# Optimization experiments

Measured on AMD Instinct MI355X. Metric: run time of the kernel, lower is better.

Reference implementation:

```python
import jax, jax.numpy as jnp
import numpy as np

MAX_CACHE_LEN = 1024
B, S, D, H = 8, 512, 512, 8
DK = D // H


def setup_inputs() -> dict:
    key = jax.random.key(0)
    ks = jax.random.split(key, 11)
    w = lambda k: jax.random.normal(k, (D, D), jnp.float32) * 0.02
    b = lambda k: jax.random.normal(k, (D,), jnp.float32) * 0.02
    return {
        "x": jax.random.normal(ks[0], (B, S, D), jnp.float32),
        "prev_k": jax.random.normal(ks[1], (B, H, MAX_CACHE_LEN, DK), jnp.float32),
        "prev_v": jax.random.normal(ks[2], (B, H, MAX_CACHE_LEN, DK), jnp.float32),
        "Wq": w(ks[3]), "bq": b(ks[4]),
        "Wk": w(ks[5]), "bk": b(ks[6]),
        "Wv": w(ks[7]), "bv": b(ks[8]),
        "Wo": w(ks[9]), "bo": b(ks[10]),
        "offset": MAX_CACHE_LEN,  # cache already full (steady-state streaming)
    }


def reference(x, prev_k, prev_v, Wq, bq, Wk, bk, Wv, bv, Wo, bo, offset):
    Bx, Sx, Dx = x.shape
    Hx = prev_k.shape[1]
    dk = Dx // Hx
    # projections (torch Linear: y = x @ W.T + b), split into heads -> [B,H,S,dk]
    def proj(W, bias):
        return (x @ W.T + bias).reshape(Bx, Sx, Hx, dk).transpose(0, 2, 1, 3)
    q = proj(Wq, bq)
    k = jnp.concatenate([prev_k, proj(Wk, bk)], axis=2)
    v = jnp.concatenate([prev_v, proj(Wv, bv)], axis=2)
    # sliding-window narrow to last MAX_CACHE_LEN keys (static shapes under jit)
    k_full = k.shape[2]
    start = max(0, k_full - MAX_CACHE_LEN)
    k = k[:, :, start:, :]
    v = v[:, :, start:, :]
    k_len = k.shape[2]
    new_offset = min(offset + Sx, MAX_CACHE_LEN)
    # scores [B,H,S,k_len]
    scores = jnp.einsum("bhqd,bhkd->bhqk", q, k) * (dk ** -0.5)
    q_start = new_offset - Sx
    q_idx = jnp.arange(Sx)[:, None] + q_start
    k_idx = jnp.arange(k_len)[None, :]
    mask = q_idx < k_idx  # future keys masked
    scores = jnp.where(mask[None, None], -jnp.inf, scores)
    attn = jax.nn.softmax(scores, axis=-1)
    out = jnp.einsum("bhqk,bhkd->bhqd", attn, v)
    out = out.transpose(0, 2, 1, 3).reshape(Bx, Sx, Dx)
    out = out @ Wo.T + bo
    return out, k, v, jnp.asarray(new_offset, jnp.int64 if jax.config.x64_enabled else jnp.int32)
```

## Files before the change

### kernel.cpp

```cpp
#include <hip/hip_runtime.h>
#include <math.h>

#define B_  8
#define S_  512
#define D_  512
#define H_  8
#define DK_ 64
#define KL_ 1024

typedef __attribute__((ext_vector_type(8))) short bf16x8;
typedef __attribute__((ext_vector_type(4))) float f32x4;

__device__ __forceinline__ unsigned short f2bf(float f) {
    unsigned u = __float_as_uint(f);
    u += 0x7FFF + ((u >> 16) & 1);
    return (unsigned short)(u >> 16);
}
__device__ __forceinline__ unsigned pkbf(float lo, float hi) {
    return __builtin_amdgcn_perm(__float_as_uint(hi), __float_as_uint(lo), 0x07060302u);
}
__device__ __forceinline__ bf16x8 pack8(float4 a, float4 b) {
    union { bf16x8 v; unsigned u[4]; } r;
    r.u[0] = pkbf(a.x, a.y); r.u[1] = pkbf(a.z, a.w);
    r.u[2] = pkbf(b.x, b.y); r.u[3] = pkbf(b.z, b.w);
    return r.v;
}
__device__ __forceinline__ void gld16(const void* g, void* l) {
    __builtin_amdgcn_global_load_lds(
        (const __attribute__((address_space(1))) unsigned int*)g,
        (__attribute__((address_space(3))) unsigned int*)l, 16, 0, 0);
}

__global__ __launch_bounds__(256)
void prep_kernel(const float4* __restrict__ pk, const float4* __restrict__ pv,
                 float4* __restrict__ kout4, float4* __restrict__ vout4,
                 float* __restrict__ off_out) {
    int i = blockIdx.x * 256 + threadIdx.x;
    int bh = i >> 13, r4 = i & 8191;
    kout4[bh * 16384 + r4] = pk[bh * 16384 + 8192 + r4];
    vout4[bh * 16384 + r4] = pv[bh * 16384 + 8192 + r4];
    if (i == 0) off_out[0] = 1024.0f;
}

template<int MODE, int BM>
__device__ __forceinline__
void mfma_gemm_body(const float* __restrict__ A32,
                    const unsigned short* __restrict__ A16,
                    const float* __restrict__ Wf,
                    const float* __restrict__ bias,
                    float* __restrict__ C32, unsigned short* __restrict__ C16) {
    constexpr int MM = BM / 32;
    __shared__ unsigned short As[BM * 32];
    __shared__ unsigned short Bs[64 * 32];
    const int t = threadIdx.x, l = t & 63, w = t >> 6;
    const int m16 = l & 15, quad = l >> 4;
    const int wm = w >> 1, wn = w & 1;
    const int bn = blockIdx.x, bm = blockIdx.y;

    f32x4 acc[MM][2] = {};

    for (int k0 = 0; k0 < 512; k0 += 32) {
        __syncthreads();
        if (MODE == 3) {
            const int h = k0 >> 6, dd0 = k0 & 63;
            const int lr = l >> 2, lc = (l & 3) * 8;
            const unsigned short* Ab =
                A16 + (((bm >> 3) * 8 + h) * 512 + (bm & 7) * 64) * 64 + dd0;
            gld16(Ab + (w * 16 + lr) * 64 + lc, &As[w * 512 + l * 8]);
        } else {
            #pragma unroll
            for (int s = 0; s < BM / 64; ++s) {
                int id = t + s * 256;
                int row = id >> 2, c8 = id & 3;
                const float* src = A32 + (bm * BM + row) * 512 + k0 + c8 * 8;
                float4 v0 = *(const float4*)src;
                float4 v1 = *(const float4*)(src + 4);
                *(bf16x8*)&As[row * 32 + c8 * 8] = pack8(v0, v1);
            }
        }
        {
            int row = t >> 2, c8 = t & 3;
            const float* src = Wf + (bn * 64 + row) * 512 + k0 + c8 * 8;
            float4 v0 = *(const float4*)src;
            float4 v1 = *(const float4*)(src + 4);
            *(bf16x8*)&Bs[row * 32 + c8 * 8] = pack8(v0, v1);
        }
        __syncthreads();

        bf16x8 af[MM], bfr[2];
        #pragma unroll
        for (int mm = 0; mm < MM; ++mm)
            af[mm] = *(const bf16x8*)&As[(wm * (BM / 2) + mm * 16 + m16) * 32 + quad * 8];
        #pragma unroll
        for (int nn = 0; nn < 2; ++nn)
            bfr[nn] = *(const bf16x8*)&Bs[(wn * 32 + nn * 16 + m16) * 32 + quad * 8];
        #pragma unroll
        for (int mm = 0; mm < MM; ++mm)
            #pragma unroll
            for (int nn = 0; nn < 2; ++nn)
                acc[mm][nn] = __builtin_amdgcn_mfma_f32_16x16x32_bf16(
                    af[mm], bfr[nn], acc[mm][nn], 0, 0, 0);
    }

    #pragma unroll
    for (int mm = 0; mm < MM; ++mm) {
        #pragma unroll
        for (int nn = 0; nn < 2; ++nn) {
            int n = bn * 64 + wn * 32 + nn * 16 + m16;
            float bv_ = bias[n];
            #pragma unroll
            for (int r = 0; r < 4; ++r) {
                int m = bm * BM + wm * (BM / 2) + mm * 16 + quad * 4 + r;
                float val = acc[mm][nn][r] + bv_;
                if (MODE == 3) {
                    C32[m * 512 + n] = val;
                } else {
                    int b = m >> 9, s = m & 511;
                    int h = n >> 6, d = n & 63;
                    if (MODE == 1) C16[((b * H_ + h) * S_ + s) * DK_ + d] = f2bf(val * 0.125f);
                    else           C32[((b * H_ + h) * KL_ + 512 + s) * DK_ + d] = val;
                }
            }
        }
    }
}

__global__ __launch_bounds__(256)
void qkv_mfma_kernel(const float* __restrict__ x,
                     const float* __restrict__ Wq, const float* __restrict__ bq,
                     const float* __restrict__ Wk, const float* __restrict__ bk,
                     const float* __restrict__ Wv, const float* __restrict__ bv,
                     unsigned short* __restrict__ Qb, float* __restrict__ kout,
                     float* __restrict__ vout) {
    if (blockIdx.z == 0)      mfma_gemm_body<1, 128>(x, nullptr, Wq, bq, nullptr, Qb);
    else if (blockIdx.z == 1) mfma_gemm_body<2, 128>(x, nullptr, Wk, bk, kout, nullptr);
    else                      mfma_gemm_body<2, 128>(x, nullptr, Wv, bv, vout, nullptr);
}

__global__ __launch_bounds__(256)
void out_mfma_kernel(const unsigned short* __restrict__ Ob, const float* __restrict__ Wo,
                     const float* __restrict__ bo, float* __restrict__ C) {
    mfma_gemm_body<3, 64>(nullptr, Ob, Wo, bo, C, nullptr);
}

__global__ __launch_bounds__(256)
void pack_kernel(const float* __restrict__ kout, const float* __restrict__ vout,
                 unsigned short* __restrict__ Kp, unsigned short* __restrict__ Vp) {
    __shared__ float Kl[64][68];
    __shared__ float Vl[64][68];
    const int kt = blockIdx.x, bh = blockIdx.y;
    const int t = threadIdx.x;
    const float* Kg = kout + (bh * KL_ + kt * 64) * DK_;
    const float* Vg = vout + (bh * KL_ + kt * 64) * DK_;
    #pragma unroll
    for (int it = 0; it < 4; ++it) {
        int idx = t + it * 256;
        int row = idx >> 4, c4 = idx & 15;
        *(float4*)&Kl[row][c4 * 4] = *(const float4*)&Kg[row * 64 + c4 * 4];
        *(float4*)&Vl[row][c4 * 4] = *(const float4*)&Vg[row * 64 + c4 * 4];
    }
    __syncthreads();
    unsigned short* Kpb = Kp + (bh * 16 + kt) * 4096;
    unsigned short* Vpb = Vp + (bh * 16 + kt) * 4096;
    #pragma unroll
    for (int s = 0; s < 2; ++s) {
        int slot = t + s * 256;
        int c = slot >> 6, l = slot & 63;
        int nn = c >> 1, hf = c & 1;
        {
            int row = nn * 16 + (l & 15), col = hf * 32 + (l >> 4) * 8;
            unsigned short tmp[8];
            #pragma unroll
            for (int j = 0; j < 8; ++j) tmp[j] = f2bf(Kl[row][col + j]);
            *(uint4*)&Kpb[c * 512 + l * 8] = *(uint4*)tmp;
        }
        {
            int row0 = hf * 32 + (l >> 4) * 8, col = nn * 16 + (l & 15);
            unsigned short tmp[8];
            #pragma unroll
            for (int j = 0; j < 8; ++j) tmp[j] = f2bf(Vl[row0 + j][col]);
            *(uint4*)&Vpb[c * 512 + l * 8] = *(uint4*)tmp;
        }
    }
}

__global__ __launch_bounds__(128)
void attn_kernel(unsigned short* qo, const unsigned short* __restrict__ Kp,
                 const unsigned short* __restrict__ Vp) {
    const int bh = blockIdx.x, qg = blockIdx.y;
    const int t = threadIdx.x, l = t & 63, w = t >> 6;
    const int m16 = l & 15, quad = l >> 4;
    const int q0 = qg * 32;

    __shared__ __attribute__((aligned(16))) unsigned short Ps[2][32][72];
    __shared__ float comb[64][40];

    bf16x8 qf[2][2];
    #pragma unroll
    for (int h = 0; h < 2; ++h)
        #pragma unroll
        for (int p = 0; p < 2; ++p)
            qf[h][p] = *(const bf16x8*)(qo + (bh * S_ + q0 + h * 16 + m16) * DK_
                                           + p * 32 + quad * 8);

    f32x4 acc[2][4] = {};
    float psum[2][4] = {};

    const int ktmax = (543 + q0) >> 6;
    const unsigned short* Kpb = Kp + (bh * 16) * 4096;
    const unsigned short* Vpb = Vp + (bh * 16) * 4096;

    for (int kt = w; kt <= ktmax; kt += 2) {
        const unsigned short* kb = Kpb + kt * 4096;
        const unsigned short* vb = Vpb + kt * 4096;
        bf16x8 kf[4][2], vf[4][2];
        #pragma unroll
        for (int nn = 0; nn < 4; ++nn)
            #pragma unroll
            for (int hf = 0; hf < 2; ++hf) {
                kf[nn][hf] = *(const bf16x8*)(kb + ((nn * 2 + hf) * 64 + l) * 8);
                vf[nn][hf] = *(const bf16x8*)(vb + ((nn * 2 + hf) * 64 + l) * 8);
            }

        f32x4 sc[2][4];
        #pragma unroll
        for (int h = 0; h < 2; ++h)
            #pragma unroll
            for (int nn = 0; nn < 4; ++nn) {
                sc[h][nn][0] = sc[h][nn][1] = sc[h][nn][2] = sc[h][nn][3] = 0.f;
                sc[h][nn] = __builtin_amdgcn_mfma_f32_16x16x32_bf16(qf[h][0], kf[nn][0], sc[h][nn], 0, 0, 0);
                sc[h][nn] = __builtin_amdgcn_mfma_f32_16x16x32_bf16(qf[h][1], kf[nn][1], sc[h][nn], 0, 0, 0);
            }

        if (kt == ktmax) {
            #pragma unroll
            for (int h = 0; h < 2; ++h)
                #pragma unroll
                for (int nn = 0; nn < 4; ++nn) {
                    int key = kt * 64 + nn * 16 + m16;
                    #pragma unroll
                    for (int r = 0; r < 4; ++r)
                        if (key > 512 + q0 + h * 16 + (quad << 2) + r)
                            sc[h][nn][r] = -INFINITY;
                }
        }

        #pragma unroll
        for (int h = 0; h < 2; ++h)
            #pragma unroll
            for (int nn = 0; nn < 4; ++nn)
                #pragma unroll
                for (int r = 0; r < 4; ++r) {
                    float p = __expf(sc[h][nn][r]);
                    psum[h][r] += p;
                    Ps[w][h * 16 + (quad << 2) + r][nn * 16 + m16] = f2bf(p);
                }

        bf16x8 pf[2][2];
        #pragma unroll
        for (int h = 0; h < 2; ++h)
            #pragma unroll
            for (int hf = 0; hf < 2; ++hf)
                pf[h][hf] = *(const bf16x8*)&Ps[w][h * 16 + m16][hf * 32 + quad * 8];
        #pragma unroll
        for (int h = 0; h < 2; ++h)
            #pragma unroll
            for (int nn = 0; nn < 4; ++nn) {
                acc[h][nn] = __builtin_amdgcn_mfma_f32_16x16x32_bf16(pf[h][0], vf[nn][0], acc[h][nn], 0, 0, 0);
                acc[h][nn] = __builtin_amdgcn_mfma_f32_16x16x32_bf16(pf[h][1], vf[nn][1], acc[h][nn], 0, 0, 0);
            }
    }

    if (w == 0) {
        #pragma unroll
        for (int h = 0; h < 2; ++h)
            #pragma unroll
            for (int nn = 0; nn < 4; ++nn)
                #pragma unroll
                for (int r = 0; r < 4; ++r)
                    comb[l][(h * 4 + nn) * 4 + r] = acc[h][nn][r];
        #pragma unroll
        for (int h = 0; h < 2; ++h)
            #pragma unroll
            for (int r = 0; r < 4; ++r)
                comb[l][32 + h * 4 + r] = psum[h][r];
    }
    __syncthreads();
    if (w == 1) {
        #pragma unroll
        for (int h = 0; h < 2; ++h)
            #pragma unroll
            for (int nn = 0; nn < 4; ++nn)
                #pragma unroll
                for (int r = 0; r < 4; ++r)
                    acc[h][nn][r] += comb[l][(h * 4 + nn) * 4 + r];
        float inv[2][4];
        #pragma unroll
        for (int h = 0; h < 2; ++h)
            #pragma unroll
            for (int r = 0; r < 4; ++r) {
                float ps = psum[h][r] + comb[l][32 + h * 4 + r];
                ps += __shfl_xor(ps, 1);
                ps += __shfl_xor(ps, 2);
                ps += __shfl_xor(ps, 4);
                ps += __shfl_xor(ps, 8);
                inv[h][r] = 1.f / ps;
            }
        unsigned short* Og = qo + (bh * S_ + q0) * DK_;
        #pragma unroll
        for (int h = 0; h < 2; ++h)
            #pragma unroll
            for (int r = 0; r < 4; ++r)
                #pragma unroll
                for (int nn = 0; nn < 4; ++nn)
                    Og[(h * 16 + (quad << 2) + r) * DK_ + nn * 16 + m16] =
                        f2bf(acc[h][nn][r] * inv[h][r]);
    }
}

extern "C" void kernel_launch(void* const* d_in, const int* in_sizes, int n_in,
                              void* d_out, int out_size, void* d_ws, size_t ws_size,
                              hipStream_t stream) {
    const float* x  = (const float*)d_in[0];
    const float* pk = (const float*)d_in[1];
    const float* pv = (const float*)d_in[2];
    const float* Wq = (const float*)d_in[3];
    const float* bq = (const float*)d_in[4];
    const float* Wk = (const float*)d_in[5];
    const float* bk = (const float*)d_in[6];
    const float* Wv = (const float*)d_in[7];
    const float* bv = (const float*)d_in[8];
    const float* Wo = (const float*)d_in[9];
    const float* bo = (const float*)d_in[10];

    float* out     = (float*)d_out;
    float* kout    = out + 2097152;
    float* vout    = kout + 4194304;
    float* off_out = vout + 4194304;

    unsigned short* Qb = (unsigned short*)d_ws;
    unsigned short* Kp = Qb + 2097152;
    unsigned short* Vp = Kp + 4194304;

    prep_kernel<<<2048, 256, 0, stream>>>((const float4*)pk, (const float4*)pv,
                                          (float4*)kout, (float4*)vout, off_out);
    qkv_mfma_kernel<<<dim3(8, 32, 3), 256, 0, stream>>>(x, Wq, bq, Wk, bk, Wv, bv,
                                                        Qb, kout, vout);
    pack_kernel<<<dim3(16, 64), 256, 0, stream>>>(kout, vout, Kp, Vp);
    attn_kernel<<<dim3(64, 16), 128, 0, stream>>>(Qb, Kp, Vp);
    out_mfma_kernel<<<dim3(8, 64), 256, 0, stream>>>(Qb, Wo, bo, out);
}
```

Measured before the change: 166.5 us.

## Pre-convert inputs to bf16, fuse K/V packing into prep and projection epilogues

The prep kernel now converts x and all four weight matrices to bf16 once, and copies the old cache half while packing it straight into the MFMA-friendly Kp/Vp layout. The K and V projection epilogues pack their new rows into Kp/Vp through shared memory, so the separate pack kernel and its full re-read of kout/vout go away. The GEMMs load bf16 tiles with direct global-to-LDS loads instead of converting fp32 on every k-step, and attention writes its output in [B,S,D] layout to a separate buffer. The cost is an extra bf16 copy of x and the weights in workspace, plus more shared memory and a block-wide sync in the K/V epilogues.

```diff
diff --git a/kernel.cpp b/kernel.cpp
--- a/kernel.cpp
+++ b/kernel.cpp
@@ -16,15 +16,6 @@
     u += 0x7FFF + ((u >> 16) & 1);
     return (unsigned short)(u >> 16);
 }
-__device__ __forceinline__ unsigned pkbf(float lo, float hi) {
-    return __builtin_amdgcn_perm(__float_as_uint(hi), __float_as_uint(lo), 0x07060302u);
-}
-__device__ __forceinline__ bf16x8 pack8(float4 a, float4 b) {
-    union { bf16x8 v; unsigned u[4]; } r;
-    r.u[0] = pkbf(a.x, a.y); r.u[1] = pkbf(a.z, a.w);
-    r.u[2] = pkbf(b.x, b.y); r.u[3] = pkbf(b.z, b.w);
-    return r.v;
-}
 __device__ __forceinline__ void gld16(const void* g, void* l) {
     __builtin_amdgcn_global_load_lds(
         (const __attribute__((address_space(1))) unsigned int*)g,
@@ -32,132 +23,56 @@
 }
 
 __global__ __launch_bounds__(256)
-void prep_kernel(const float4* __restrict__ pk, const float4* __restrict__ pv,
-                 float4* __restrict__ kout4, float4* __restrict__ vout4,
+void prep_kernel(const float* __restrict__ x,
+                 const float* __restrict__ Wq, const float* __restrict__ Wk,
+                 const float* __restrict__ Wv, const float* __restrict__ Wo,
+                 const float* __restrict__ pk, const float* __restrict__ pv,
+                 unsigned short* __restrict__ xb,
+                 unsigned short* __restrict__ Wqb, unsigned short* __restrict__ Wkb,
+                 unsigned short* __restrict__ Wvb, unsigned short* __restrict__ Wob,
+                 float* __restrict__ kout, float* __restrict__ vout,
+                 unsigned short* __restrict__ Kp, unsigned short* __restrict__ Vp,
                  float* __restrict__ off_out) {
-    int i = blockIdx.x * 256 + threadIdx.x;
-    int bh = i >> 13, r4 = i & 8191;
-    kout4[bh * 16384 + r4] = pk[bh * 16384 + 8192 + r4];
-    vout4[bh * 16384 + r4] = pv[bh * 16384 + 8192 + r4];
-    if (i == 0) off_out[0] = 1024.0f;
-}
-
-template<int MODE, int BM>
-__device__ __forceinline__
-void mfma_gemm_body(const float* __restrict__ A32,
-                    const unsigned short* __restrict__ A16,
-                    const float* __restrict__ Wf,
-                    const float* __restrict__ bias,
-                    float* __restrict__ C32, unsigned short* __restrict__ C16) {
-    constexpr int MM = BM / 32;
-    __shared__ unsigned short As[BM * 32];
-    __shared__ unsigned short Bs[64 * 32];
-    const int t = threadIdx.x, l = t & 63, w = t >> 6;
-    const int m16 = l & 15, quad = l >> 4;
-    const int wm = w >> 1, wn = w & 1;
-    const int bn = blockIdx.x, bm = blockIdx.y;
-
-    f32x4 acc[MM][2] = {};
-
-    for (int k0 = 0; k0 < 512; k0 += 32) {
-        __syncthreads();
-        if (MODE == 3) {
-            const int h = k0 >> 6, dd0 = k0 & 63;
-            const int lr = l >> 2, lc = (l & 3) * 8;
-            const unsigned short* Ab =
-                A16 + (((bm >> 3) * 8 + h) * 512 + (bm & 7) * 64) * 64 + dd0;
-            gld16(Ab + (w * 16 + lr) * 64 + lc, &As[w * 512 + l * 8]);
+    const int blk = blockIdx.x, t = threadIdx.x;
+    if (blk == 0 && t == 0) off_out[0] = 1024.0f;
+
+    if (blk < 1536) {
+        const float* src; unsigned short* dst; int off;
+        if (blk < 1024) {
+            src = x; dst = xb; off = blk * 256 + t;
         } else {
-            #pragma unroll
-            for (int s = 0; s < BM / 64; ++s) {
-                int id = t + s * 256;
-                int row = id >> 2, c8 = id & 3;
-                const float* src = A32 + (bm * BM + row) * 512 + k0 + c8 * 8;
-                float4 v0 = *(const float4*)src;
-                float4 v1 = *(const float4*)(src + 4);
-                *(bf16x8*)&As[row * 32 + c8 * 8] = pack8(v0, v1);
-            }
-        }
-        {
-            int row = t >> 2, c8 = t & 3;
-            const float* src = Wf + (bn * 64 + row) * 512 + k0 + c8 * 8;
-            float4 v0 = *(const float4*)src;
-            float4 v1 = *(const float4*)(src + 4);
-            *(bf16x8*)&Bs[row * 32 + c8 * 8] = pack8(v0, v1);
-        }
-        __syncthreads();
-
-        bf16x8 af[MM], bfr[2];
-        #pragma unroll
-        for (int mm = 0; mm < MM; ++mm)
-            af[mm] = *(const bf16x8*)&As[(wm * (BM / 2) + mm * 16 + m16) * 32 + quad * 8];
-        #pragma unroll
-        for (int nn = 0; nn < 2; ++nn)
-            bfr[nn] = *(const bf16x8*)&Bs[(wn * 32 + nn * 16 + m16) * 32 + quad * 8];
-        #pragma unroll
-        for (int mm = 0; mm < MM; ++mm)
-            #pragma unroll
-            for (int nn = 0; nn < 2; ++nn)
-                acc[mm][nn] = __builtin_amdgcn_mfma_f32_16x16x32_bf16(
-                    af[mm], bfr[nn], acc[mm][nn], 0, 0, 0);
-    }
-
-    #pragma unroll
-    for (int mm = 0; mm < MM; ++mm) {
-        #pragma unroll
-        for (int nn = 0; nn < 2; ++nn) {
-            int n = bn * 64 + wn * 32 + nn * 16 + m16;
-            float bv_ = bias[n];
-            #pragma unroll
-            for (int r = 0; r < 4; ++r) {
-                int m = bm * BM + wm * (BM / 2) + mm * 16 + quad * 4 + r;
-                float val = acc[mm][nn][r] + bv_;
-                if (MODE == 3) {
-                    C32[m * 512 + n] = val;
-                } else {
-                    int b = m >> 9, s = m & 511;
-                    int h = n >> 6, d = n & 63;
-                    if (MODE == 1) C16[((b * H_ + h) * S_ + s) * DK_ + d] = f2bf(val * 0.125f);
-                    else           C32[((b * H_ + h) * KL_ + 512 + s) * DK_ + d] = val;
-                }
-            }
-        }
-    }
-}
-
-__global__ __launch_bounds__(256)
-void qkv_mfma_kernel(const float* __restrict__ x,
-                     const float* __restrict__ Wq, const float* __restrict__ bq,
-                     const float* __restrict__ Wk, const float* __restrict__ bk,
-                     const float* __restrict__ Wv, const float* __restrict__ bv,
-                     unsigned short* __restrict__ Qb, float* __restrict__ kout,
-                     float* __restrict__ vout) {
-    if (blockIdx.z == 0)      mfma_gemm_body<1, 128>(x, nullptr, Wq, bq, nullptr, Qb);
-    else if (blockIdx.z == 1) mfma_gemm_body<2, 128>(x, nullptr, Wk, bk, kout, nullptr);
-    else                      mfma_gemm_body<2, 128>(x, nullptr, Wv, bv, vout, nullptr);
-}
-
-__global__ __launch_bounds__(256)
-void out_mfma_kernel(const unsigned short* __restrict__ Ob, const float* __restrict__ Wo,
-                     const float* __restrict__ bo, float* __restrict__ C) {
-    mfma_gemm_body<3, 64>(nullptr, Ob, Wo, bo, C, nullptr);
-}
-
-__global__ __launch_bounds__(256)
-void pack_kernel(const float* __restrict__ kout, const float* __restrict__ vout,
-                 unsigned short* __restrict__ Kp, unsigned short* __restrict__ Vp) {
+            int widx = blk - 1024;
+            int grp = widx >> 7, wb = widx & 127;
+            const float* ws_[4]        = {Wq, Wk, Wv, Wo};
+            unsigned short* wd_[4]     = {Wqb, Wkb, Wvb, Wob};
+            src = ws_[grp]; dst = wd_[grp]; off = wb * 256 + t;
+        }
+        float4 v0 = ((const float4*)src)[off * 2];
+        float4 v1 = ((const float4*)src)[off * 2 + 1];
+        unsigned short tmp[8] = {f2bf(v0.x), f2bf(v0.y), f2bf(v0.z), f2bf(v0.w),
+                                 f2bf(v1.x), f2bf(v1.y), f2bf(v1.z), f2bf(v1.w)};
+        *(uint4*)&dst[off * 8] = *(uint4*)tmp;
+        return;
+    }
+
     __shared__ float Kl[64][68];
     __shared__ float Vl[64][68];
-    const int kt = blockIdx.x, bh = blockIdx.y;
-    const int t = threadIdx.x;
-    const float* Kg = kout + (bh * KL_ + kt * 64) * DK_;
-    const float* Vg = vout + (bh * KL_ + kt * 64) * DK_;
+    const int pb = blk - 1536;
+    const int kt = pb & 7, bh = pb >> 3;
+    const float* Kg = pk + (bh * KL_ + 512 + kt * 64) * DK_;
+    const float* Vg = pv + (bh * KL_ + 512 + kt * 64) * DK_;
+    float* Ko = kout + (bh * KL_ + kt * 64) * DK_;
+    float* Vo = vout + (bh * KL_ + kt * 64) * DK_;
     #pragma unroll
     for (int it = 0; it < 4; ++it) {
         int idx = t + it * 256;
         int row = idx >> 4, c4 = idx & 15;
-        *(float4*)&Kl[row][c4 * 4] = *(const float4*)&Kg[row * 64 + c4 * 4];
-        *(float4*)&Vl[row][c4 * 4] = *(const float4*)&Vg[row * 64 + c4 * 4];
+        float4 kv = *(const float4*)&Kg[row * 64 + c4 * 4];
+        float4 vv = *(const float4*)&Vg[row * 64 + c4 * 4];
+        *(float4*)&Ko[row * 64 + c4 * 4] = kv;
+        *(float4*)&Vo[row * 64 + c4 * 4] = vv;
+        *(float4*)&Kl[row][c4 * 4] = kv;
+        *(float4*)&Vl[row][c4 * 4] = vv;
     }
     __syncthreads();
     unsigned short* Kpb = Kp + (bh * 16 + kt) * 4096;
@@ -184,9 +99,135 @@
     }
 }
 
+template<int MODE, int BM>
+__device__ __forceinline__
+void mfma_gemm_body(const unsigned short* __restrict__ A,
+                    const unsigned short* __restrict__ Wb,
+                    const float* __restrict__ bias,
+                    float* __restrict__ C32, unsigned short* __restrict__ C16,
+                    unsigned short* __restrict__ Pk) {
+    constexpr int MM = BM / 32;
+    __shared__ unsigned short As[BM * 32];
+    __shared__ unsigned short Bs[64 * 32];
+    const int t = threadIdx.x, l = t & 63, w = t >> 6;
+    const int m16 = l & 15, quad = l >> 4;
+    const int wm = w >> 1, wn = w & 1;
+    const int bn = blockIdx.x, bm = blockIdx.y;
+    const int lr = l >> 2, lc = (l & 3) * 8;
+
+    f32x4 acc[MM][2] = {};
+    const unsigned short* Ag = A + (bm * BM) * 512;
+    const unsigned short* Wg = Wb + (bn * 64) * 512;
+
+    for (int k0 = 0; k0 < 512; k0 += 32) {
+        __syncthreads();
+        #pragma unroll
+        for (int q = 0; q < BM / 64; ++q) {
+            int chunk = w * (BM / 64) + q;
+            gld16(Ag + (chunk * 16 + lr) * 512 + k0 + lc, &As[chunk * 512 + l * 8]);
+        }
+        gld16(Wg + (w * 16 + lr) * 512 + k0 + lc, &Bs[w * 512 + l * 8]);
+        __syncthreads();
+
+        bf16x8 af[MM], bfr[2];
+        #pragma unroll
+        for (int mm = 0; mm < MM; ++mm)
+            af[mm] = *(const bf16x8*)&As[(wm * (BM / 2) + mm * 16 + m16) * 32 + quad * 8];
+        #pragma unroll
+        for (int nn = 0; nn < 2; ++nn)
+            bfr[nn] = *(const bf16x8*)&Bs[(wn * 32 + nn * 16 + m16) * 32 + quad * 8];
+        #pragma unroll
+        for (int mm = 0; mm < MM; ++mm)
+            #pragma unroll
+            for (int nn = 0; nn < 2; ++nn)
+                acc[mm][nn] = __builtin_amdgcn_mfma_f32_16x16x32_bf16(
+                    af[mm], bfr[nn], acc[mm][nn], 0, 0, 0);
+    }
+
+    if constexpr (MODE == 2 || MODE == 4) {
+        __shared__ __attribute__((aligned(16))) unsigned short Ts[9216];
+        #pragma unroll
+        for (int mm = 0; mm < MM; ++mm)
+            #pragma unroll
+            for (int nn = 0; nn < 2; ++nn) {
+                int n = bn * 64 + wn * 32 + nn * 16 + m16;
+                float bv_ = bias[n];
+                int d = n & 63;
+                #pragma unroll
+                for (int r = 0; r < 4; ++r) {
+                    int ml = wm * (BM / 2) + mm * 16 + quad * 4 + r;
+                    int m = bm * BM + ml;
+                    float val = acc[mm][nn][r] + bv_;
+                    int b = m >> 9, s = m & 511, h = n >> 6;
+                    C32[((b * H_ + h) * KL_ + 512 + s) * DK_ + d] = val;
+                    if (MODE == 2) Ts[ml * 72 + d]  = f2bf(val);
+                    else           Ts[d * 136 + ml] = f2bf(val);
+                }
+            }
+        __syncthreads();
+        const int bh = (bm >> 2) * H_ + bn;
+        const int kt0 = 8 + (bm & 3) * 2;
+        #pragma unroll
+        for (int T = 0; T < 2; ++T)
+            #pragma unroll
+            for (int cp = 0; cp < 2; ++cp) {
+                int c = w * 2 + cp, nn = c >> 1, hf = c & 1;
+                uint4 frag;
+                if (MODE == 2)
+                    frag = *(const uint4*)&Ts[(T * 64 + nn * 16 + (l & 15)) * 72
+                                              + hf * 32 + (l >> 4) * 8];
+                else
+                    frag = *(const uint4*)&Ts[(nn * 16 + (l & 15)) * 136
+                                              + T * 64 + hf * 32 + (l >> 4) * 8];
+                *(uint4*)&Pk[((bh * 16 + kt0 + T) * 4096) + c * 512 + l * 8] = frag;
+            }
+    } else {
+        #pragma unroll
+        for (int mm = 0; mm < MM; ++mm)
+            #pragma unroll
+            for (int nn = 0; nn < 2; ++nn) {
+                int n = bn * 64 + wn * 32 + nn * 16 + m16;
+                float bv_ = bias[n];
+                #pragma unroll
+                for (int r = 0; r < 4; ++r) {
+                    int m = bm * BM + wm * (BM / 2) + mm * 16 + quad * 4 + r;
+                    float val = acc[mm][nn][r] + bv_;
+                    if (MODE == 3) {
+                        C32[m * 512 + n] = val;
+                    } else {
+                        int b = m >> 9, s = m & 511;
+                        int h = n >> 6, d = n & 63;
+                        C16[((b * H_ + h) * S_ + s) * DK_ + d] = f2bf(val * 0.125f);
+                    }
+                }
+            }
+    }
+}
+
+__global__ __launch_bounds__(256)
+void qkv_mfma_kernel(const unsigned short* __restrict__ xb,
+                     const unsigned short* __restrict__ Wqb, const float* __restrict__ bq,
+                     const unsigned short* __restrict__ Wkb, const float* __restrict__ bk,
+                     const unsigned short* __restrict__ Wvb, const float* __restrict__ bv,
+                     unsigned short* __restrict__ Qb, float* __restrict__ kout,
+                     float* __restrict__ vout,
+                     unsigned short* __restrict__ Kp, unsigned short* __restrict__ Vp) {
+    if (blockIdx.z == 0)      mfma_gemm_body<1, 128>(xb, Wqb, bq, nullptr, Qb, nullptr);
+    else if (blockIdx.z == 1) mfma_gemm_body<2, 128>(xb, Wkb, bk, kout, nullptr, Kp);
+    else                      mfma_gemm_body<4, 128>(xb, Wvb, bv, vout, nullptr, Vp);
+}
+
+__global__ __launch_bounds__(256)
+void out_mfma_kernel(const unsigned short* __restrict__ Ob, const unsigned short* __restrict__ Wob,
+                     const float* __restrict__ bo, float* __restrict__ C) {
+    mfma_gemm_body<3, 64>(Ob, Wob, bo, C, nullptr, nullptr);
+}
+
 __global__ __launch_bounds__(128)
-void attn_kernel(unsigned short* qo, const unsigned short* __restrict__ Kp,
-                 const unsigned short* __restrict__ Vp) {
+void attn_kernel(const unsigned short* __restrict__ Qb,
+                 const unsigned short* __restrict__ Kp,
+                 const unsigned short* __restrict__ Vp,
+                 unsigned short* __restrict__ Ob) {
     const int bh = blockIdx.x, qg = blockIdx.y;
     const int t = threadIdx.x, l = t & 63, w = t >> 6;
     const int m16 = l & 15, quad = l >> 4;
@@ -197,11 +238,11 @@
 
     bf16x8 qf[2][2];
     #pragma unroll
-    for (int h = 0; h < 2; ++h)
+    for (int qh = 0; qh < 2; ++qh)
         #pragma unroll
         for (int p = 0; p < 2; ++p)
-            qf[h][p] = *(const bf16x8*)(qo + (bh * S_ + q0 + h * 16 + m16) * DK_
-                                           + p * 32 + quad * 8);
+            qf[qh][p] = *(const bf16x8*)(Qb + (bh * S_ + q0 + qh * 16 + m16) * DK_
+                                            + p * 32 + quad * 8);
 
     f32x4 acc[2][4] = {};
     float psum[2][4] = {};
@@ -224,97 +265,97 @@
 
         f32x4 sc[2][4];
         #pragma unroll
-        for (int h = 0; h < 2; ++h)
+        for (int qh = 0; qh < 2; ++qh)
             #pragma unroll
             for (int nn = 0; nn < 4; ++nn) {
-                sc[h][nn][0] = sc[h][nn][1] = sc[h][nn][2] = sc[h][nn][3] = 0.f;
-                sc[h][nn] = __builtin_amdgcn_mfma_f32_16x16x32_bf16(qf[h][0], kf[nn][0], sc[h][nn], 0, 0, 0);
-                sc[h][nn] = __builtin_amdgcn_mfma_f32_16x16x32_bf16(qf[h][1], kf[nn][1], sc[h][nn], 0, 0, 0);
+                sc[qh][nn][0] = sc[qh][nn][1] = sc[qh][nn][2] = sc[qh][nn][3] = 0.f;
+                sc[qh][nn] = __builtin_amdgcn_mfma_f32_16x16x32_bf16(qf[qh][0], kf[nn][0], sc[qh][nn], 0, 0, 0);
+                sc[qh][nn] = __builtin_amdgcn_mfma_f32_16x16x32_bf16(qf[qh][1], kf[nn][1], sc[qh][nn], 0, 0, 0);
             }
 
         if (kt == ktmax) {
             #pragma unroll
-            for (int h = 0; h < 2; ++h)
+            for (int qh = 0; qh < 2; ++qh)
                 #pragma unroll
                 for (int nn = 0; nn < 4; ++nn) {
                     int key = kt * 64 + nn * 16 + m16;
                     #pragma unroll
                     for (int r = 0; r < 4; ++r)
-                        if (key > 512 + q0 + h * 16 + (quad << 2) + r)
-                            sc[h][nn][r] = -INFINITY;
+                        if (key > 512 + q0 + qh * 16 + (quad << 2) + r)
+                            sc[qh][nn][r] = -INFINITY;
                 }
         }
 
         #pragma unroll
-        for (int h = 0; h < 2; ++h)
+        for (int qh = 0; qh < 2; ++qh)
             #pragma unroll
             for (int nn = 0; nn < 4; ++nn)
                 #pragma unroll
                 for (int r = 0; r < 4; ++r) {
-                    float p = __expf(sc[h][nn][r]);
-                    psum[h][r] += p;
-                    Ps[w][h * 16 + (quad << 2) + r][nn * 16 + m16] = f2bf(p);
+                    float p = __expf(sc[qh][nn][r]);
+                    psum[qh][r] += p;
+                    Ps[w][qh * 16 + (quad << 2) + r][nn * 16 + m16] = f2bf(p);
                 }
 
         bf16x8 pf[2][2];
         #pragma unroll
-        for (int h = 0; h < 2; ++h)
+        for (int qh = 0; qh < 2; ++qh)
             #pragma unroll
             for (int hf = 0; hf < 2; ++hf)
-                pf[h][hf] = *(const bf16x8*)&Ps[w][h * 16 + m16][hf * 32 + quad * 8];
-        #pragma unroll
-        for (int h = 0; h < 2; ++h)
+                pf[qh][hf] = *(const bf16x8*)&Ps[w][qh * 16 + m16][hf * 32 + quad * 8];
+        #pragma unroll
+        for (int qh = 0; qh < 2; ++qh)
             #pragma unroll
             for (int nn = 0; nn < 4; ++nn) {
-                acc[h][nn] = __builtin_amdgcn_mfma_f32_16x16x32_bf16(pf[h][0], vf[nn][0], acc[h][nn], 0, 0, 0);
-                acc[h][nn] = __builtin_amdgcn_mfma_f32_16x16x32_bf16(pf[h][1], vf[nn][1], acc[h][nn], 0, 0, 0);
+                acc[qh][nn] = __builtin_amdgcn_mfma_f32_16x16x32_bf16(pf[qh][0], vf[nn][0], acc[qh][nn], 0, 0, 0);
+                acc[qh][nn] = __builtin_amdgcn_mfma_f32_16x16x32_bf16(pf[qh][1], vf[nn][1], acc[qh][nn], 0, 0, 0);
             }
     }
 
     if (w == 0) {
         #pragma unroll
-        for (int h = 0; h < 2; ++h)
+        for (int qh = 0; qh < 2; ++qh)
             #pragma unroll
             for (int nn = 0; nn < 4; ++nn)
                 #pragma unroll
                 for (int r = 0; r < 4; ++r)
-                    comb[l][(h * 4 + nn) * 4 + r] = acc[h][nn][r];
-        #pragma unroll
-        for (int h = 0; h < 2; ++h)
+                    comb[l][(qh * 4 + nn) * 4 + r] = acc[qh][nn][r];
+        #pragma unroll
+        for (int qh = 0; qh < 2; ++qh)
             #pragma unroll
             for (int r = 0; r < 4; ++r)
-                comb[l][32 + h * 4 + r] = psum[h][r];
+                comb[l][32 + qh * 4 + r] = psum[qh][r];
     }
     __syncthreads();
     if (w == 1) {
         #pragma unroll
-        for (int h = 0; h < 2; ++h)
+        for (int qh = 0; qh < 2; ++qh)
             #pragma unroll
             for (int nn = 0; nn < 4; ++nn)
                 #pragma unroll
                 for (int r = 0; r < 4; ++r)
-                    acc[h][nn][r] += comb[l][(h * 4 + nn) * 4 + r];
+                    acc[qh][nn][r] += comb[l][(qh * 4 + nn) * 4 + r];
         float inv[2][4];
         #pragma unroll
-        for (int h = 0; h < 2; ++h)
+        for (int qh = 0; qh < 2; ++qh)
             #pragma unroll
             for (int r = 0; r < 4; ++r) {
-                float ps = psum[h][r] + comb[l][32 + h * 4 + r];
+                float ps = psum[qh][r] + comb[l][32 + qh * 4 + r];
                 ps += __shfl_xor(ps, 1);
                 ps += __shfl_xor(ps, 2);
                 ps += __shfl_xor(ps, 4);
                 ps += __shfl_xor(ps, 8);
-                inv[h][r] = 1.f / ps;
-            }
-        unsigned short* Og = qo + (bh * S_ + q0) * DK_;
-        #pragma unroll
-        for (int h = 0; h < 2; ++h)
+                inv[qh][r] = 1.f / ps;
+            }
+        unsigned short* Og = Ob + ((bh >> 3) * S_ + q0) * D_ + (bh & 7) * DK_;
+        #pragma unroll
+        for (int qh = 0; qh < 2; ++qh)
             #pragma unroll
             for (int r = 0; r < 4; ++r)
                 #pragma unroll
                 for (int nn = 0; nn < 4; ++nn)
-                    Og[(h * 16 + (quad << 2) + r) * DK_ + nn * 16 + m16] =
-                        f2bf(acc[h][nn][r] * inv[h][r]);
+                    Og[(qh * 16 + (quad << 2) + r) * D_ + nn * 16 + m16] =
+                        f2bf(acc[qh][nn][r] * inv[qh][r]);
     }
 }
 
@@ -338,15 +379,21 @@
     float* vout    = kout + 4194304;
     float* off_out = vout + 4194304;
 
-    unsigned short* Qb = (unsigned short*)d_ws;
-    unsigned short* Kp = Qb + 2097152;
-    unsigned short* Vp = Kp + 4194304;
-
-    prep_kernel<<<2048, 256, 0, stream>>>((const float4*)pk, (const float4*)pv,
-                                          (float4*)kout, (float4*)vout, off_out);
-    qkv_mfma_kernel<<<dim3(8, 32, 3), 256, 0, stream>>>(x, Wq, bq, Wk, bk, Wv, bv,
-                                                        Qb, kout, vout);
-    pack_kernel<<<dim3(16, 64), 256, 0, stream>>>(kout, vout, Kp, Vp);
-    attn_kernel<<<dim3(64, 16), 128, 0, stream>>>(Qb, Kp, Vp);
-    out_mfma_kernel<<<dim3(8, 64), 256, 0, stream>>>(Qb, Wo, bo, out);
-}
+    unsigned short* xb  = (unsigned short*)d_ws;
+    unsigned short* Wqb = xb + 2097152;
+    unsigned short* Wkb = Wqb + 262144;
+    unsigned short* Wvb = Wkb + 262144;
+    unsigned short* Wob = Wvb + 262144;
+    unsigned short* Qb  = Wob + 262144;
+    unsigned short* Kp  = Qb + 2097152;
+    unsigned short* Vp  = Kp + 4194304;
+    unsigned short* Ob  = xb;
+
+    prep_kernel<<<2048, 256, 0, stream>>>(x, Wq, Wk, Wv, Wo, pk, pv,
+                                          xb, Wqb, Wkb, Wvb, Wob,
+                                          kout, vout, Kp, Vp, off_out);
+    qkv_mfma_kernel<<<dim3(8, 32, 3), 256, 0, stream>>>(xb, Wqb, bq, Wkb, bk, Wvb, bv,
+                                                        Qb, kout, vout, Kp, Vp);
+    attn_kernel<<<dim3(64, 16), 128, 0, stream>>>(Qb, Kp, Vp, Ob);
+    out_mfma_kernel<<<dim3(8, 64), 256, 0, stream>>>(Ob, Wob, bo, out);
+}
```

Measured after the change: 165.0 us. About the same (-0.9%).
